# Optimization experiments

Measured on AMD Instinct MI355X. Metric: run time of the kernel, lower is better.

## Reference

```python
import jax, jax.numpy as jnp
import numpy as np

IMG, P, CIN, D, NH, NB, NC = 512, 16, 3, 384, 4, 3, 2
HD = D // NH
NP_ = (IMG // P) ** 2
T = NP_ + 1
FF = 4 * D


def _ln(x, s, b, eps=1e-5):
    m = x.mean(-1, keepdims=True)
    v = ((x - m) ** 2).mean(-1, keepdims=True)
    return (x - m) / jnp.sqrt(v + eps) * s + b


def setup_inputs() -> dict:
    key = jax.random.key(0)
    ks = jax.random.split(key, 20)
    s = 0.02
    inp = {
        'x': jax.random.normal(ks[0], (16, CIN, IMG, IMG), jnp.float32),
        'targets': jax.random.randint(ks[1], (16,), 0, NC),
        'conv_w': jax.random.normal(ks[2], (D, CIN, P, P), jnp.float32) * s,
        'conv_b': jnp.zeros((D,), jnp.float32),
        'cls_token': jax.random.normal(ks[3], (1, 1, D), jnp.float32),
        'pos_emb': jax.random.normal(ks[4], (T, D), jnp.float32) * s,
        'ln1_s': jnp.ones((NB, D), jnp.float32), 'ln1_b': jnp.zeros((NB, D), jnp.float32),
        'ln2_s': jnp.ones((NB, D), jnp.float32), 'ln2_b': jnp.zeros((NB, D), jnp.float32),
        'wq': jax.random.normal(ks[5], (NB, D, D), jnp.float32) * s,
        'wk': jax.random.normal(ks[6], (NB, D, D), jnp.float32) * s,
        'wv': jax.random.normal(ks[7], (NB, D, D), jnp.float32) * s,
        'wo': jax.random.normal(ks[8], (NB, D, D), jnp.float32) * s,
        'bo': jnp.zeros((NB, D), jnp.float32),
        'w1': jax.random.normal(ks[9], (NB, D, FF), jnp.float32) * s,
        'b1': jnp.zeros((NB, FF), jnp.float32),
        'w2': jax.random.normal(ks[10], (NB, FF, D), jnp.float32) * s,
        'b2': jnp.zeros((NB, D), jnp.float32),
        'lnf_s': jnp.ones((D,), jnp.float32), 'lnf_b': jnp.zeros((D,), jnp.float32),
        'proj_w': jax.random.normal(ks[11], (D, NC), jnp.float32) * s,
        'proj_b': jnp.zeros((NC,), jnp.float32),
    }
    return inp


def _forward(x, conv_w, conv_b, cls_token, pos_emb, ln1_s, ln1_b, ln2_s, ln2_b,
             wq, wk, wv, wo, bo, w1, b1, w2, b2, lnf_s, lnf_b, proj_w, proj_b):
    B = x.shape[0]
    # patch embedding: conv with kernel==stride == non-overlapping patches
    xp = x.reshape(B, CIN, IMG // P, P, IMG // P, P)
    pe = jnp.einsum('bchpwq,dcpq->bhwd', xp, conv_w).reshape(B, NP_, D) + conv_b
    h = jnp.concatenate([jnp.broadcast_to(cls_token, (B, 1, D)), pe], axis=1)  # (B,T,D)
    h = h + pos_emb
    scale = HD ** (-0.5)
    for i in range(NB):
        hn = _ln(h, ln1_s[i], ln1_b[i])
        q = (hn @ wq[i]).reshape(B, T, NH, HD).transpose(0, 2, 1, 3)
        k = (hn @ wk[i]).reshape(B, T, NH, HD).transpose(0, 2, 1, 3)
        v = (hn @ wv[i]).reshape(B, T, NH, HD).transpose(0, 2, 1, 3)
        # cdist p=2 (Euclidean distance) attention scores
        d2 = (jnp.sum(q * q, -1)[..., :, None] + jnp.sum(k * k, -1)[..., None, :]
              - 2.0 * jnp.einsum('bhqd,bhkd->bhqk', q, k))
        wei = jax.nn.softmax(jnp.sqrt(jnp.maximum(d2, 0.0)) * scale, axis=-1)
        vals = jnp.einsum('bhqk,bhkd->bhqd', wei, v).transpose(0, 2, 1, 3).reshape(B, T, D)
        h = h + vals @ wo[i] + bo[i]
        hn2 = _ln(h, ln2_s[i], ln2_b[i])
        h = h + jax.nn.relu(hn2 @ w1[i] + b1[i]) @ w2[i] + b2[i]
    h = _ln(h, lnf_s, lnf_b)
    logits = h @ proj_w + proj_b
    return logits[:, 0]  # (B, NC) cls-token logits


def reference(x, targets, conv_w, conv_b, cls_token, pos_emb, ln1_s, ln1_b, ln2_s, ln2_b,
              wq, wk, wv, wo, bo, w1, b1, w2, b2, lnf_s, lnf_b, proj_w, proj_b):
    cls_logits = _forward(x, conv_w, conv_b, cls_token, pos_emb, ln1_s, ln1_b, ln2_s, ln2_b,
                          wq, wk, wv, wo, bo, w1, b1, w2, b2, lnf_s, lnf_b, proj_w, proj_b)
    logp = jax.nn.log_softmax(cls_logits, axis=-1)
    loss = -jnp.mean(jnp.take_along_axis(logp, targets[:, None], axis=1))
    return (cls_logits, loss)
```

## Files before the change

### kernel.cpp

```cpp
#include <hip/hip_runtime.h>
#include <math.h>


#define BATCH   16
#define TSEQ    1025
#define DMODEL  384
#define NHEAD   4
#define HDIM    96
#define NBLK    3
#define FFDIM   1536
#define IMGSZ   512
#define NPATCHI 1024
#define MROWS   (BATCH*TSEQ)
#define MPATCH  (BATCH*NPATCHI)
#define KPE     768
#define VTS     1088
#define ATT_SCALE 0.10206207261596577f

typedef __attribute__((ext_vector_type(8))) __bf16 bf16x8;
typedef __attribute__((ext_vector_type(4))) float  f32x4;

__device__ __forceinline__ f32x4 fzero4() {
  f32x4 v; v[0] = 0.f; v[1] = 0.f; v[2] = 0.f; v[3] = 0.f; return v;
}
__device__ __forceinline__ bf16x8 bzero8() {
  bf16x8 v;
#pragma unroll
  for (int j = 0; j < 8; ++j) v[j] = (__bf16)0.f;
  return v;
}

template<int EPI>
__global__ __launch_bounds__(256, 2) void mgemm_k(
    const __bf16* __restrict__ A, const __bf16* __restrict__ Bt,
    const float* __restrict__ bias, const float* __restrict__ res,
    float* __restrict__ Cf, __bf16* __restrict__ Cb, int M, int N, int K)
{
  __shared__ __bf16 Al[2][128][40];
  __shared__ __bf16 Bl[2][128][40];
  const int tid = threadIdx.x;
  const int lane = tid & 63;
  const int w = tid >> 6;
  const int wr = w >> 1, wc = w & 1;
  const int l15 = lane & 15, g = lane >> 4;
  const int row0 = blockIdx.x * 128, col0 = blockIdx.y * 128;
  const int srow = tid >> 1, soff = (tid & 1) * 16;
  int ar = row0 + srow; if (ar > M - 1) ar = M - 1;
  const __bf16* ap = A + (size_t)ar * K + soff;
  const __bf16* bp = Bt + (size_t)(col0 + srow) * K + soff;

  f32x4 acc[4][4];
#pragma unroll
  for (int i = 0; i < 4; ++i)
#pragma unroll
    for (int j = 0; j < 4; ++j) acc[i][j] = fzero4();

  const int nk = K >> 5;
  bf16x8 ra0 = *(const bf16x8*)ap;
  bf16x8 ra1 = *(const bf16x8*)(ap + 8);
  bf16x8 rb0 = *(const bf16x8*)bp;
  bf16x8 rb1 = *(const bf16x8*)(bp + 8);
  *(bf16x8*)&Al[0][srow][soff]     = ra0;
  *(bf16x8*)&Al[0][srow][soff + 8] = ra1;
  *(bf16x8*)&Bl[0][srow][soff]     = rb0;
  *(bf16x8*)&Bl[0][srow][soff + 8] = rb1;
  __syncthreads();
  int cur = 0;
  for (int kt = 0; kt < nk; ++kt) {
    const bool pf = (kt + 1 < nk);
    if (pf) {
      const __bf16* a2 = ap + (size_t)(kt + 1) * 32;
      const __bf16* b2 = bp + (size_t)(kt + 1) * 32;
      ra0 = *(const bf16x8*)a2; ra1 = *(const bf16x8*)(a2 + 8);
      rb0 = *(const bf16x8*)b2; rb1 = *(const bf16x8*)(b2 + 8);
    }
    bf16x8 af[4], bfr[4];
#pragma unroll
    for (int mi = 0; mi < 4; ++mi)
      af[mi] = *(const bf16x8*)&Al[cur][wr * 64 + mi * 16 + l15][g * 8];
#pragma unroll
    for (int ni = 0; ni < 4; ++ni)
      bfr[ni] = *(const bf16x8*)&Bl[cur][wc * 64 + ni * 16 + l15][g * 8];
#pragma unroll
    for (int mi = 0; mi < 4; ++mi)
#pragma unroll
      for (int ni = 0; ni < 4; ++ni)
        acc[mi][ni] = __builtin_amdgcn_mfma_f32_16x16x32_bf16(
            af[mi], bfr[ni], acc[mi][ni], 0, 0, 0);
    if (pf) {
      *(bf16x8*)&Al[cur ^ 1][srow][soff]     = ra0;
      *(bf16x8*)&Al[cur ^ 1][srow][soff + 8] = ra1;
      *(bf16x8*)&Bl[cur ^ 1][srow][soff]     = rb0;
      *(bf16x8*)&Bl[cur ^ 1][srow][soff + 8] = rb1;
    }
    __syncthreads();
    cur ^= 1;
  }
#pragma unroll
  for (int ni = 0; ni < 4; ++ni) {
    const int gc = col0 + wc * 64 + ni * 16 + l15;
    const float bv = (EPI & 1) ? bias[gc] : 0.f;
#pragma unroll
    for (int mi = 0; mi < 4; ++mi) {
#pragma unroll
      for (int r = 0; r < 4; ++r) {
        const int gr = row0 + wr * 64 + mi * 16 + g * 4 + r;
        if (gr >= M) continue;
        float v = acc[mi][ni][r] + bv;
        if (EPI & 2) v = fmaxf(v, 0.f);
        if (EPI & 4) v += res[(size_t)gr * N + gc];
        if (EPI & 8)  Cf[(size_t)gr * N + gc] = v;
        if (EPI & 16) Cb[(size_t)gr * N + gc] = (__bf16)v;
      }
    }
  }
}

__global__ void vtr_k(const __bf16* __restrict__ qkv, __bf16* __restrict__ Vt)
{
  __shared__ __bf16 t[32][33];
  const int bh = blockIdx.z;
  const int bb = bh >> 2, hh = bh & 3;
  const int t0 = blockIdx.x * 32;
  const int d0 = blockIdx.y * 32;
  const int tx = threadIdx.x, ty = threadIdx.y;
#pragma unroll
  for (int i = 0; i < 4; ++i) {
    const int tt = t0 + ty + 8 * i;
    t[ty + 8 * i][tx] = (tt < TSEQ)
        ? qkv[(size_t)(bb * TSEQ + tt) * 1152 + 768 + hh * 96 + d0 + tx]
        : (__bf16)0.f;
  }
  __syncthreads();
#pragma unroll
  for (int i = 0; i < 4; ++i)
    Vt[((size_t)bh * 96 + d0 + ty + 8 * i) * VTS + t0 + tx] = t[tx][ty + 8 * i];
}

__global__ __launch_bounds__(256, 4) void attn_k(
    const __bf16* __restrict__ qkv, const __bf16* __restrict__ Vtg,
    const float* __restrict__ sq2, const float* __restrict__ sk2,
    __bf16* __restrict__ O)
{
  __shared__ __bf16 Kl[64][104];
  __shared__ __bf16 Vl[96][72];
  __shared__ __bf16 Pl[64][72];
  const int qt = blockIdx.x, bh = blockIdx.y;
  const int bb = bh >> 2, hh = bh & 3;
  const int tid = threadIdx.x;
  const int w = tid >> 6, lane = tid & 63;
  const int l15 = lane & 15, g = lane >> 4;
  const int q0 = qt * 64 + w * 16;
  const float* sq2h = sq2 + (size_t)bh * TSEQ;
  const float* sk2h = sk2 + (size_t)bh * TSEQ;
  const __bf16* vbase = Vtg + (size_t)bh * 96 * VTS;

  bf16x8 qf[3];
  float sqv[4];
  {
    int qr = q0 + l15; if (qr > TSEQ - 1) qr = TSEQ - 1;
    const __bf16* qp = qkv + (size_t)(bb * TSEQ + qr) * 1152 + hh * 96 + g * 8;
#pragma unroll
    for (int kf = 0; kf < 3; ++kf) qf[kf] = *(const bf16x8*)(qp + kf * 32);
#pragma unroll
    for (int r = 0; r < 4; ++r) {
      int qq = q0 + g * 4 + r; if (qq > TSEQ - 1) qq = TSEQ - 1;
      sqv[r] = sq2h[qq];
    }
  }

  float mrun[4], lrun[4];
  f32x4 accO[6];
#pragma unroll
  for (int r = 0; r < 4; ++r) { mrun[r] = -INFINITY; lrun[r] = 0.f; }
#pragma unroll
  for (int n = 0; n < 6; ++n) accO[n] = fzero4();

  bf16x8 kr[3], vr[3];
  auto load_chunk = [&](int c) {
    const int kbase = c * 64;
#pragma unroll
    for (int i = 0; i < 3; ++i) {
      const int idx = tid + i * 256;
      const int row = idx / 12, cc = idx - row * 12;
      const int kg = kbase + row;
      kr[i] = (kg < TSEQ)
          ? *(const bf16x8*)(qkv + (size_t)(bb * TSEQ + kg) * 1152 + 384
                             + hh * 96 + cc * 8)
          : bzero8();
      const int d = idx >> 3, o8 = (idx & 7) * 8;
      vr[i] = *(const bf16x8*)(vbase + (size_t)d * VTS + kbase + o8);
    }
  };

  load_chunk(0);

  for (int c = 0; c < 17; ++c) {
    const int kbase = c * 64;
    __syncthreads();
#pragma unroll
    for (int i = 0; i < 3; ++i) {
      const int idx = tid + i * 256;
      const int row = idx / 12, cc = idx - row * 12;
      *(bf16x8*)&Kl[row][cc * 8] = kr[i];
      const int d = idx >> 3, o8 = (idx & 7) * 8;
      *(bf16x8*)&Vl[d][o8] = vr[i];
    }
    __syncthreads();
    if (c + 1 < 17) load_chunk(c + 1);

    f32x4 sf[4];
#pragma unroll
    for (int ks = 0; ks < 4; ++ks) sf[ks] = fzero4();
    __builtin_amdgcn_s_setprio(1);
#pragma unroll
    for (int ks = 0; ks < 4; ++ks) {
      bf16x8 kb0 = *(const bf16x8*)&Kl[ks * 16 + l15][g * 8];
      bf16x8 kb1 = *(const bf16x8*)&Kl[ks * 16 + l15][32 + g * 8];
      bf16x8 kb2 = *(const bf16x8*)&Kl[ks * 16 + l15][64 + g * 8];
      sf[ks] = __builtin_amdgcn_mfma_f32_16x16x32_bf16(qf[0], kb0, sf[ks], 0, 0, 0);
      sf[ks] = __builtin_amdgcn_mfma_f32_16x16x32_bf16(qf[1], kb1, sf[ks], 0, 0, 0);
      sf[ks] = __builtin_amdgcn_mfma_f32_16x16x32_bf16(qf[2], kb2, sf[ks], 0, 0, 0);
    }
    __builtin_amdgcn_s_setprio(0);

    float nmax[4] = {-INFINITY, -INFINITY, -INFINITY, -INFINITY};
#pragma unroll
    for (int ks = 0; ks < 4; ++ks) {
      const int kgl = kbase + ks * 16 + l15;
      const bool kvld = (kgl < TSEQ);
      const float kv2 = sk2h[kvld ? kgl : 0];
#pragma unroll
      for (int r = 0; r < 4; ++r) {
        const float d2 = sqv[r] + kv2 - 2.f * sf[ks][r];
        const float s = kvld ? sqrtf(fmaxf(d2, 0.f)) * ATT_SCALE : -INFINITY;
        sf[ks][r] = s;
        nmax[r] = fmaxf(nmax[r], s);
      }
    }
#pragma unroll
    for (int r = 0; r < 4; ++r) {
      float v = nmax[r];
      v = fmaxf(v, __shfl_xor(v, 1, 64));
      v = fmaxf(v, __shfl_xor(v, 2, 64));
      v = fmaxf(v, __shfl_xor(v, 4, 64));
      v = fmaxf(v, __shfl_xor(v, 8, 64));
      const float mn = fmaxf(mrun[r], v);
      const float f = __expf(mrun[r] - mn);
      mrun[r] = mn;
      lrun[r] *= f;
#pragma unroll
      for (int n = 0; n < 6; ++n) accO[n][r] *= f;
    }
    float ps[4] = {0.f, 0.f, 0.f, 0.f};
#pragma unroll
    for (int ks = 0; ks < 4; ++ks)
#pragma unroll
      for (int r = 0; r < 4; ++r) {
        const float p = __expf(sf[ks][r] - mrun[r]);
        ps[r] += p;
        Pl[w * 16 + g * 4 + r][ks * 16 + l15] = (__bf16)p;
      }
#pragma unroll
    for (int r = 0; r < 4; ++r) {
      float v = ps[r];
      v += __shfl_xor(v, 1, 64);
      v += __shfl_xor(v, 2, 64);
      v += __shfl_xor(v, 4, 64);
      v += __shfl_xor(v, 8, 64);
      lrun[r] += v;
    }

    __builtin_amdgcn_s_setprio(1);
#pragma unroll
    for (int ks2 = 0; ks2 < 2; ++ks2) {
      bf16x8 pa = *(const bf16x8*)&Pl[w * 16 + l15][ks2 * 32 + g * 8];
#pragma unroll
      for (int n = 0; n < 6; ++n) {
        bf16x8 vb = *(const bf16x8*)&Vl[n * 16 + l15][ks2 * 32 + g * 8];
        accO[n] = __builtin_amdgcn_mfma_f32_16x16x32_bf16(pa, vb, accO[n], 0, 0, 0);
      }
    }
    __builtin_amdgcn_s_setprio(0);
  }

#pragma unroll
  for (int r = 0; r < 4; ++r) {
    const int qr = q0 + g * 4 + r;
    if (qr >= TSEQ) continue;
    const float inv = 1.f / lrun[r];
#pragma unroll
    for (int n = 0; n < 6; ++n)
      O[(size_t)(bb * TSEQ + qr) * 384 + hh * 96 + n * 16 + l15] =
          (__bf16)(accO[n][r] * inv);
  }
}

__global__ __launch_bounds__(256) void im2col_k(
    const float* __restrict__ x, __bf16* __restrict__ Ai)
{
  const int i = blockIdx.x * 256 + threadIdx.x;
  const int row = i / 96;
  const int k = (i - row * 96) * 8;
  const int b = row >> 10;
  const int pidx = row & 1023;
  const int py = pidx >> 5, px = pidx & 31;
  const int cc = k >> 8;
  const int rem = k & 255;
  const int p = rem >> 4, q = rem & 15;
  const float* src = x + ((size_t)((b * 3 + cc) * IMGSZ + py * 16 + p)) * IMGSZ
                       + px * 16 + q;
  const float4 a = *(const float4*)src;
  const float4 c4 = *(const float4*)(src + 4);
  bf16x8 o;
  o[0] = (__bf16)a.x;  o[1] = (__bf16)a.y;  o[2] = (__bf16)a.z;  o[3] = (__bf16)a.w;
  o[4] = (__bf16)c4.x; o[5] = (__bf16)c4.y; o[6] = (__bf16)c4.z; o[7] = (__bf16)c4.w;
  *(bf16x8*)&Ai[(size_t)i * 8] = o;
}

__global__ void wt_k(const float* __restrict__ src, size_t srcZ,
                     __bf16* __restrict__ dst, size_t dstZ, int K, int N)
{
  __shared__ float t[32][33];
  const float* s = src + blockIdx.z * srcZ;
  __bf16* d = dst + blockIdx.z * dstZ;
  const int k0 = blockIdx.x * 32, n0 = blockIdx.y * 32;
  const int tx = threadIdx.x, ty = threadIdx.y;
#pragma unroll
  for (int i = 0; i < 4; ++i)
    t[ty + 8 * i][tx] = s[(size_t)(k0 + ty + 8 * i) * N + n0 + tx];
  __syncthreads();
#pragma unroll
  for (int i = 0; i < 4; ++i)
    d[(size_t)(n0 + ty + 8 * i) * K + k0 + tx] = (__bf16)t[tx][ty + 8 * i];
}

__global__ void cvt_k(const float* __restrict__ src, __bf16* __restrict__ dst, int n8)
{
  const int i = blockIdx.x * 256 + threadIdx.x;
  if (i >= n8) return;
  const float4 a = *(const float4*)&src[(size_t)i * 8];
  const float4 b = *(const float4*)&src[(size_t)i * 8 + 4];
  bf16x8 o;
  o[0] = (__bf16)a.x; o[1] = (__bf16)a.y; o[2] = (__bf16)a.z; o[3] = (__bf16)a.w;
  o[4] = (__bf16)b.x; o[5] = (__bf16)b.y; o[6] = (__bf16)b.z; o[7] = (__bf16)b.w;
  *(bf16x8*)&dst[(size_t)i * 8] = o;
}

__global__ __launch_bounds__(256) void embed_k(
    const float* __restrict__ pe, const float* __restrict__ cls,
    const float* __restrict__ pos, float* __restrict__ h)
{
  const int i = blockIdx.x * 256 + threadIdx.x;
  const int row = i / 96;
  const int d4 = (i - row * 96) * 4;
  const int b = row / TSEQ;
  const int t = row - b * TSEQ;
  const float4 po = *(const float4*)&pos[(size_t)t * DMODEL + d4];
  float4 r;
  if (t == 0) {
    const float4 cv = *(const float4*)&cls[d4];
    r = make_float4(cv.x + po.x, cv.y + po.y, cv.z + po.z, cv.w + po.w);
  } else {
    const float4 pv = *(const float4*)&pe[((size_t)(b * NPATCHI + t - 1)) * DMODEL + d4];
    r = make_float4(pv.x + po.x, pv.y + po.y, pv.z + po.z, pv.w + po.w);
  }
  *(float4*)&h[(size_t)row * DMODEL + d4] = r;
}

__global__ __launch_bounds__(256) void ln_k(
    const float* __restrict__ in, const float* __restrict__ sc,
    const float* __restrict__ bi, __bf16* __restrict__ out)
{
  const int w = threadIdx.x >> 6, lane = threadIdx.x & 63;
  const int row = blockIdx.x * 4 + w;
  const float* r = in + (size_t)row * DMODEL;
  float v[6], sum = 0.f, ss = 0.f;
#pragma unroll
  for (int j = 0; j < 6; ++j) {
    const float xv = r[lane + 64 * j];
    v[j] = xv; sum += xv; ss += xv * xv;
  }
#pragma unroll
  for (int m = 1; m < 64; m <<= 1) {
    sum += __shfl_xor(sum, m, 64);
    ss  += __shfl_xor(ss,  m, 64);
  }
  const float mean = sum * (1.f / 384.f);
  const float var  = ss * (1.f / 384.f) - mean * mean;
  const float rstd = rsqrtf(var + 1e-5f);
  __bf16* o = out + (size_t)row * DMODEL;
#pragma unroll
  for (int j = 0; j < 6; ++j) {
    const int col = lane + 64 * j;
    o[col] = (__bf16)((v[j] - mean) * rstd * sc[col] + bi[col]);
  }
}

__global__ __launch_bounds__(256) void sumsq_k(
    const __bf16* __restrict__ qkv, float* __restrict__ sq2,
    float* __restrict__ sk2)
{
  const int w = threadIdx.x >> 6, lane = threadIdx.x & 63;
  const int row = blockIdx.x * 4 + w;
  const int h = lane >> 4, lg = lane & 15;
  const __bf16* q = qkv + (size_t)row * 1152 + h * HDIM;
  float s1 = 0.f, s2 = 0.f;
#pragma unroll
  for (int j = 0; j < 6; ++j) {
    const float a = (float)q[lg + 16 * j];
    const float c = (float)q[384 + lg + 16 * j];
    s1 += a * a; s2 += c * c;
  }
#pragma unroll
  for (int m = 1; m < 16; m <<= 1) {
    s1 += __shfl_xor(s1, m, 64);
    s2 += __shfl_xor(s2, m, 64);
  }
  if (lg == 0) {
    const int b = row / TSEQ, t = row - b * TSEQ;
    sq2[((size_t)b * NHEAD + h) * TSEQ + t] = s1;
    sk2[((size_t)b * NHEAD + h) * TSEQ + t] = s2;
  }
}

__global__ __launch_bounds__(256) void head_k(
    const float* __restrict__ h, const float* __restrict__ gs,
    const float* __restrict__ gb, const float* __restrict__ pw,
    const float* __restrict__ pb, const int* __restrict__ tgt,
    float* __restrict__ out)
{
  __shared__ float lg[BATCH][2];
  const int w = threadIdx.x >> 6, lane = threadIdx.x & 63;
  for (int b = w; b < BATCH; b += 4) {
    const float* r = h + (size_t)b * TSEQ * DMODEL;
    float v[6], sum = 0.f, ss = 0.f;
#pragma unroll
    for (int j = 0; j < 6; ++j) {
      const float xv = r[lane + 64 * j];
      v[j] = xv; sum += xv; ss += xv * xv;
    }
#pragma unroll
    for (int m = 1; m < 64; m <<= 1) {
      sum += __shfl_xor(sum, m, 64);
      ss  += __shfl_xor(ss,  m, 64);
    }
    const float mean = sum * (1.f / 384.f);
    const float var  = ss * (1.f / 384.f) - mean * mean;
    const float rstd = rsqrtf(var + 1e-5f);
    float l0 = 0.f, l1 = 0.f;
#pragma unroll
    for (int j = 0; j < 6; ++j) {
      const int col = lane + 64 * j;
      const float hnv = (v[j] - mean) * rstd * gs[col] + gb[col];
      l0 = fmaf(hnv, pw[col * 2 + 0], l0);
      l1 = fmaf(hnv, pw[col * 2 + 1], l1);
    }
#pragma unroll
    for (int m = 1; m < 64; m <<= 1) {
      l0 += __shfl_xor(l0, m, 64);
      l1 += __shfl_xor(l1, m, 64);
    }
    if (lane == 0) { lg[b][0] = l0 + pb[0]; lg[b][1] = l1 + pb[1]; }
  }
  __syncthreads();
  if (threadIdx.x < 32)
    out[threadIdx.x] = lg[threadIdx.x >> 1][threadIdx.x & 1];
  if (threadIdx.x == 0) {
    float acc = 0.f;
    for (int b = 0; b < BATCH; ++b) {
      const float a = lg[b][0], c = lg[b][1];
      const float mx = fmaxf(a, c);
      const float lse = mx + logf(expf(a - mx) + expf(c - mx));
      const float lp = ((tgt[b] == 0) ? a : c) - lse;
      acc += lp;
    }
    out[32] = -acc * (1.f / BATCH);
  }
}

extern "C" void kernel_launch(void* const* d_in, const int* in_sizes, int n_in,
                              void* d_out, int out_size, void* d_ws, size_t ws_size,
                              hipStream_t stream)
{
  const float* x       = (const float*)d_in[0];
  const int*   targets = (const int*)  d_in[1];
  const float* conv_w  = (const float*)d_in[2];
  const float* conv_b  = (const float*)d_in[3];
  const float* cls_tok = (const float*)d_in[4];
  const float* pos_emb = (const float*)d_in[5];
  const float* ln1_s   = (const float*)d_in[6];
  const float* ln1_b   = (const float*)d_in[7];
  const float* ln2_s   = (const float*)d_in[8];
  const float* ln2_b   = (const float*)d_in[9];
  const float* wq      = (const float*)d_in[10];
  const float* wk      = (const float*)d_in[11];
  const float* wv      = (const float*)d_in[12];
  const float* wo      = (const float*)d_in[13];
  const float* bo      = (const float*)d_in[14];
  const float* w1      = (const float*)d_in[15];
  const float* b1      = (const float*)d_in[16];
  const float* w2      = (const float*)d_in[17];
  const float* b2      = (const float*)d_in[18];
  const float* lnf_s   = (const float*)d_in[19];
  const float* lnf_b   = (const float*)d_in[20];
  const float* proj_w  = (const float*)d_in[21];
  const float* proj_b  = (const float*)d_in[22];

  char* p = (char*)d_ws;
  auto alloc = [&](size_t bytes) -> void* {
    void* r = (void*)p; p += (bytes + 255) & ~(size_t)255; return r;
  };
  float*  h     = (float*) alloc((size_t)MROWS * DMODEL * 4);
  __bf16* hn    = (__bf16*)alloc((size_t)MROWS * DMODEL * 2);
  __bf16* qkv   = (__bf16*)alloc((size_t)MROWS * 1152 * 2);
  __bf16* Obuf  = (__bf16*)alloc((size_t)MROWS * DMODEL * 2);
  float*  pe    = (float*) alloc((size_t)MPATCH * DMODEL * 4);
  float*  sq2   = (float*) alloc((size_t)BATCH * NHEAD * TSEQ * 4);
  float*  sk2   = (float*) alloc((size_t)BATCH * NHEAD * TSEQ * 4);
  __bf16* cwb   = (__bf16*)alloc((size_t)DMODEL * KPE * 2);
  __bf16* wqkvT = (__bf16*)alloc((size_t)NBLK * 1152 * DMODEL * 2);
  __bf16* woT   = (__bf16*)alloc((size_t)NBLK * DMODEL * DMODEL * 2);
  __bf16* w1T   = (__bf16*)alloc((size_t)NBLK * FFDIM * DMODEL * 2);
  __bf16* w2T   = (__bf16*)alloc((size_t)NBLK * DMODEL * FFDIM * 2);
  if ((size_t)(p - (char*)d_ws) > ws_size) return;
  __bf16* Ai  = qkv;
  __bf16* ffb = qkv;
  __bf16* Vtg = (__bf16*)pe;

  cvt_k<<<144, 256, 0, stream>>>(conv_w, cwb, (DMODEL * KPE) / 8);
  {
    dim3 blk(32, 8);
    wt_k<<<dim3(12, 12, 3), blk, 0, stream>>>(wq, (size_t)DMODEL * DMODEL,
        wqkvT + 0,               (size_t)1152 * DMODEL, DMODEL, DMODEL);
    wt_k<<<dim3(12, 12, 3), blk, 0, stream>>>(wk, (size_t)DMODEL * DMODEL,
        wqkvT + 384 * DMODEL,    (size_t)1152 * DMODEL, DMODEL, DMODEL);
    wt_k<<<dim3(12, 12, 3), blk, 0, stream>>>(wv, (size_t)DMODEL * DMODEL,
        wqkvT + 768 * DMODEL,    (size_t)1152 * DMODEL, DMODEL, DMODEL);
    wt_k<<<dim3(12, 12, 3), blk, 0, stream>>>(wo, (size_t)DMODEL * DMODEL,
        woT, (size_t)DMODEL * DMODEL, DMODEL, DMODEL);
    wt_k<<<dim3(12, 48, 3), blk, 0, stream>>>(w1, (size_t)DMODEL * FFDIM,
        w1T, (size_t)FFDIM * DMODEL, DMODEL, FFDIM);
    wt_k<<<dim3(48, 12, 3), blk, 0, stream>>>(w2, (size_t)FFDIM * DMODEL,
        w2T, (size_t)DMODEL * FFDIM, FFDIM, DMODEL);
  }

  im2col_k<<<6144, 256, 0, stream>>>(x, Ai);
  mgemm_k<9><<<dim3(128, 3), 256, 0, stream>>>(
      Ai, cwb, conv_b, nullptr, pe, nullptr, MPATCH, DMODEL, KPE);
  embed_k<<<6150, 256, 0, stream>>>(pe, cls_tok, pos_emb, h);

  for (int i = 0; i < NBLK; ++i) {
    ln_k<<<4100, 256, 0, stream>>>(h, ln1_s + i * DMODEL, ln1_b + i * DMODEL, hn);
    mgemm_k<16><<<dim3(129, 9), 256, 0, stream>>>(
        hn, wqkvT + (size_t)i * 1152 * DMODEL, nullptr, nullptr,
        nullptr, qkv, MROWS, 1152, DMODEL);
    sumsq_k<<<4100, 256, 0, stream>>>(qkv, sq2, sk2);
    vtr_k<<<dim3(34, 3, 64), dim3(32, 8), 0, stream>>>(qkv, Vtg);
    attn_k<<<dim3(17, 64), 256, 0, stream>>>(qkv, Vtg, sq2, sk2, Obuf);
    mgemm_k<13><<<dim3(129, 3), 256, 0, stream>>>(
        Obuf, woT + (size_t)i * DMODEL * DMODEL, bo + i * DMODEL, h,
        h, nullptr, MROWS, DMODEL, DMODEL);
    ln_k<<<4100, 256, 0, stream>>>(h, ln2_s + i * DMODEL, ln2_b + i * DMODEL, hn);
    mgemm_k<19><<<dim3(129, 12), 256, 0, stream>>>(
        hn, w1T + (size_t)i * FFDIM * DMODEL, b1 + i * FFDIM, nullptr,
        nullptr, ffb, MROWS, FFDIM, DMODEL);
    mgemm_k<13><<<dim3(129, 3), 256, 0, stream>>>(
        ffb, w2T + (size_t)i * DMODEL * FFDIM, b2 + i * DMODEL, h,
        h, nullptr, MROWS, DMODEL, FFDIM);
  }

  head_k<<<1, 256, 0, stream>>>(h, lnf_s, lnf_b, proj_w, proj_b, targets,
                                (float*)d_out);
}
```

Before: 1.296 ms.

## Use direct global-to-LDS loads in GEMM and register-fed lazy-rescale attention

The GEMM now stages tiles with global_load_lds straight into unpadded LDS, dropping the register round-trip, and raises occupancy to 4 blocks per SM. The attention kernel no longer stages K and V through LDS; each wave loads its K and V fragments from global memory into registers. Online softmax rescaling is skipped unless a row max grows by more than 8. The row sum comes from an appended ones-row in Vt, computed by a seventh MFMA column tile. The cost is redundant global traffic per wave and wasted MFMA work on the padding rows, and the unpadded LDS layout may cause bank conflicts. GEMM rows are no longer clamped to M, so the last partial tile reads past the end of A.

```diff
diff --git a/kernel.cpp b/kernel.cpp
--- a/kernel.cpp
+++ b/kernel.cpp
@@ -15,39 +15,41 @@
 #define MPATCH  (BATCH*NPATCHI)
 #define KPE     768
 #define VTS     1088
+#define VROWS   112
 #define ATT_SCALE 0.10206207261596577f
 
 typedef __attribute__((ext_vector_type(8))) __bf16 bf16x8;
 typedef __attribute__((ext_vector_type(4))) float  f32x4;
+typedef unsigned int u32;
 
 __device__ __forceinline__ f32x4 fzero4() {
   f32x4 v; v[0] = 0.f; v[1] = 0.f; v[2] = 0.f; v[3] = 0.f; return v;
 }
-__device__ __forceinline__ bf16x8 bzero8() {
-  bf16x8 v;
-#pragma unroll
-  for (int j = 0; j < 8; ++j) v[j] = (__bf16)0.f;
-  return v;
+
+__device__ __forceinline__ void gl_lds16(const __bf16* g, __bf16* l) {
+  __builtin_amdgcn_global_load_lds(
+      (const __attribute__((address_space(1))) u32*)g,
+      (__attribute__((address_space(3))) u32*)l, 16, 0, 0);
 }
 
 template<int EPI>
-__global__ __launch_bounds__(256, 2) void mgemm_k(
+__global__ __launch_bounds__(256, 4) void mgemm_k(
     const __bf16* __restrict__ A, const __bf16* __restrict__ Bt,
     const float* __restrict__ bias, const float* __restrict__ res,
     float* __restrict__ Cf, __bf16* __restrict__ Cb, int M, int N, int K)
 {
-  __shared__ __bf16 Al[2][128][40];
-  __shared__ __bf16 Bl[2][128][40];
+  __shared__ __bf16 Al[2][128][32];
+  __shared__ __bf16 Bl[2][128][32];
   const int tid = threadIdx.x;
   const int lane = tid & 63;
   const int w = tid >> 6;
   const int wr = w >> 1, wc = w & 1;
   const int l15 = lane & 15, g = lane >> 4;
   const int row0 = blockIdx.x * 128, col0 = blockIdx.y * 128;
-  const int srow = tid >> 1, soff = (tid & 1) * 16;
-  int ar = row0 + srow; if (ar > M - 1) ar = M - 1;
-  const __bf16* ap = A + (size_t)ar * K + soff;
-  const __bf16* bp = Bt + (size_t)(col0 + srow) * K + soff;
+  const int sr = w * 32 + (lane >> 2);
+  const int sc = (lane & 3) * 8;
+  const __bf16* Ab = A  + (size_t)(row0 + sr) * K + sc;
+  const __bf16* Bb = Bt + (size_t)(col0 + sr) * K + sc;
 
   f32x4 acc[4][4];
 #pragma unroll
@@ -56,24 +58,19 @@
     for (int j = 0; j < 4; ++j) acc[i][j] = fzero4();
 
   const int nk = K >> 5;
-  bf16x8 ra0 = *(const bf16x8*)ap;
-  bf16x8 ra1 = *(const bf16x8*)(ap + 8);
-  bf16x8 rb0 = *(const bf16x8*)bp;
-  bf16x8 rb1 = *(const bf16x8*)(bp + 8);
-  *(bf16x8*)&Al[0][srow][soff]     = ra0;
-  *(bf16x8*)&Al[0][srow][soff + 8] = ra1;
-  *(bf16x8*)&Bl[0][srow][soff]     = rb0;
-  *(bf16x8*)&Bl[0][srow][soff + 8] = rb1;
+  auto stage = [&](int buf, int kt) {
+#pragma unroll
+    for (int j = 0; j < 2; ++j) {
+      gl_lds16(Ab + (size_t)(j * 16) * K + kt * 32, &Al[buf][w * 32 + j * 16][0]);
+      gl_lds16(Bb + (size_t)(j * 16) * K + kt * 32, &Bl[buf][w * 32 + j * 16][0]);
+    }
+  };
+
+  stage(0, 0);
   __syncthreads();
   int cur = 0;
   for (int kt = 0; kt < nk; ++kt) {
-    const bool pf = (kt + 1 < nk);
-    if (pf) {
-      const __bf16* a2 = ap + (size_t)(kt + 1) * 32;
-      const __bf16* b2 = bp + (size_t)(kt + 1) * 32;
-      ra0 = *(const bf16x8*)a2; ra1 = *(const bf16x8*)(a2 + 8);
-      rb0 = *(const bf16x8*)b2; rb1 = *(const bf16x8*)(b2 + 8);
-    }
+    if (kt + 1 < nk) stage(cur ^ 1, kt + 1);
     bf16x8 af[4], bfr[4];
 #pragma unroll
     for (int mi = 0; mi < 4; ++mi)
@@ -81,18 +78,14 @@
 #pragma unroll
     for (int ni = 0; ni < 4; ++ni)
       bfr[ni] = *(const bf16x8*)&Bl[cur][wc * 64 + ni * 16 + l15][g * 8];
+    __builtin_amdgcn_s_setprio(1);
 #pragma unroll
     for (int mi = 0; mi < 4; ++mi)
 #pragma unroll
       for (int ni = 0; ni < 4; ++ni)
         acc[mi][ni] = __builtin_amdgcn_mfma_f32_16x16x32_bf16(
             af[mi], bfr[ni], acc[mi][ni], 0, 0, 0);
-    if (pf) {
-      *(bf16x8*)&Al[cur ^ 1][srow][soff]     = ra0;
-      *(bf16x8*)&Al[cur ^ 1][srow][soff + 8] = ra1;
-      *(bf16x8*)&Bl[cur ^ 1][srow][soff]     = rb0;
-      *(bf16x8*)&Bl[cur ^ 1][srow][soff + 8] = rb1;
-    }
+    __builtin_amdgcn_s_setprio(0);
     __syncthreads();
     cur ^= 1;
   }
@@ -124,6 +117,16 @@
   const int t0 = blockIdx.x * 32;
   const int d0 = blockIdx.y * 32;
   const int tx = threadIdx.x, ty = threadIdx.y;
+  if (d0 >= 96) {
+#pragma unroll
+    for (int i = 0; i < 4; ++i) {
+      const int d = d0 + ty + 8 * i;
+      if (d < VROWS)
+        Vt[((size_t)bh * VROWS + d) * VTS + t0 + tx] =
+            (d == 96) ? (__bf16)1.f : (__bf16)0.f;
+    }
+    return;
+  }
 #pragma unroll
   for (int i = 0; i < 4; ++i) {
     const int tt = t0 + ty + 8 * i;
@@ -134,16 +137,14 @@
   __syncthreads();
 #pragma unroll
   for (int i = 0; i < 4; ++i)
-    Vt[((size_t)bh * 96 + d0 + ty + 8 * i) * VTS + t0 + tx] = t[tx][ty + 8 * i];
-}
-
-__global__ __launch_bounds__(256, 4) void attn_k(
+    Vt[((size_t)bh * VROWS + d0 + ty + 8 * i) * VTS + t0 + tx] = t[tx][ty + 8 * i];
+}
+
+__global__ __launch_bounds__(256, 3) void attn_k(
     const __bf16* __restrict__ qkv, const __bf16* __restrict__ Vtg,
     const float* __restrict__ sq2, const float* __restrict__ sk2,
     __bf16* __restrict__ O)
 {
-  __shared__ __bf16 Kl[64][104];
-  __shared__ __bf16 Vl[96][72];
   __shared__ __bf16 Pl[64][72];
   const int qt = blockIdx.x, bh = blockIdx.y;
   const int bb = bh >> 2, hh = bh & 3;
@@ -153,7 +154,8 @@
   const int q0 = qt * 64 + w * 16;
   const float* sq2h = sq2 + (size_t)bh * TSEQ;
   const float* sk2h = sk2 + (size_t)bh * TSEQ;
-  const __bf16* vbase = Vtg + (size_t)bh * 96 * VTS;
+  const __bf16* kbp = qkv + (size_t)bb * TSEQ * 1152 + 384 + hh * 96;
+  const __bf16* vbp = Vtg + (size_t)bh * VROWS * VTS;
 
   bf16x8 qf[3];
   float sqv[4];
@@ -169,62 +171,44 @@
     }
   }
 
-  float mrun[4], lrun[4];
-  f32x4 accO[6];
-#pragma unroll
-  for (int r = 0; r < 4; ++r) { mrun[r] = -INFINITY; lrun[r] = 0.f; }
-#pragma unroll
-  for (int n = 0; n < 6; ++n) accO[n] = fzero4();
-
-  bf16x8 kr[3], vr[3];
-  auto load_chunk = [&](int c) {
-    const int kbase = c * 64;
-#pragma unroll
-    for (int i = 0; i < 3; ++i) {
-      const int idx = tid + i * 256;
-      const int row = idx / 12, cc = idx - row * 12;
-      const int kg = kbase + row;
-      kr[i] = (kg < TSEQ)
-          ? *(const bf16x8*)(qkv + (size_t)(bb * TSEQ + kg) * 1152 + 384
-                             + hh * 96 + cc * 8)
-          : bzero8();
-      const int d = idx >> 3, o8 = (idx & 7) * 8;
-      vr[i] = *(const bf16x8*)(vbase + (size_t)d * VTS + kbase + o8);
-    }
-  };
-
-  load_chunk(0);
+  float mrun[4];
+  f32x4 accO[7];
+#pragma unroll
+  for (int r = 0; r < 4; ++r) mrun[r] = -INFINITY;
+#pragma unroll
+  for (int n = 0; n < 7; ++n) accO[n] = fzero4();
 
   for (int c = 0; c < 17; ++c) {
     const int kbase = c * 64;
-    __syncthreads();
-#pragma unroll
-    for (int i = 0; i < 3; ++i) {
-      const int idx = tid + i * 256;
-      const int row = idx / 12, cc = idx - row * 12;
-      *(bf16x8*)&Kl[row][cc * 8] = kr[i];
-      const int d = idx >> 3, o8 = (idx & 7) * 8;
-      *(bf16x8*)&Vl[d][o8] = vr[i];
-    }
-    __syncthreads();
-    if (c + 1 < 17) load_chunk(c + 1);
 
     f32x4 sf[4];
 #pragma unroll
     for (int ks = 0; ks < 4; ++ks) sf[ks] = fzero4();
-    __builtin_amdgcn_s_setprio(1);
-#pragma unroll
-    for (int ks = 0; ks < 4; ++ks) {
-      bf16x8 kb0 = *(const bf16x8*)&Kl[ks * 16 + l15][g * 8];
-      bf16x8 kb1 = *(const bf16x8*)&Kl[ks * 16 + l15][32 + g * 8];
-      bf16x8 kb2 = *(const bf16x8*)&Kl[ks * 16 + l15][64 + g * 8];
-      sf[ks] = __builtin_amdgcn_mfma_f32_16x16x32_bf16(qf[0], kb0, sf[ks], 0, 0, 0);
-      sf[ks] = __builtin_amdgcn_mfma_f32_16x16x32_bf16(qf[1], kb1, sf[ks], 0, 0, 0);
-      sf[ks] = __builtin_amdgcn_mfma_f32_16x16x32_bf16(qf[2], kb2, sf[ks], 0, 0, 0);
-    }
-    __builtin_amdgcn_s_setprio(0);
-
-    float nmax[4] = {-INFINITY, -INFINITY, -INFINITY, -INFINITY};
+    {
+      bf16x8 kb[4][3];
+#pragma unroll
+      for (int ks = 0; ks < 4; ++ks) {
+        int krow = kbase + ks * 16 + l15; if (krow > TSEQ - 1) krow = TSEQ - 1;
+        const __bf16* kp = kbp + (size_t)krow * 1152 + g * 8;
+#pragma unroll
+        for (int kf = 0; kf < 3; ++kf) kb[ks][kf] = *(const bf16x8*)(kp + kf * 32);
+      }
+      __builtin_amdgcn_s_setprio(1);
+#pragma unroll
+      for (int ks = 0; ks < 4; ++ks)
+#pragma unroll
+        for (int kf = 0; kf < 3; ++kf)
+          sf[ks] = __builtin_amdgcn_mfma_f32_16x16x32_bf16(
+              qf[kf], kb[ks][kf], sf[ks], 0, 0, 0);
+      __builtin_amdgcn_s_setprio(0);
+    }
+
+    bf16x8 vb0[7];
+#pragma unroll
+    for (int n = 0; n < 7; ++n)
+      vb0[n] = *(const bf16x8*)(vbp + (size_t)(n * 16 + l15) * VTS + kbase + g * 8);
+
+    float cm[4] = {-INFINITY, -INFINITY, -INFINITY, -INFINITY};
 #pragma unroll
     for (int ks = 0; ks < 4; ++ks) {
       const int kgl = kbase + ks * 16 + l15;
@@ -235,52 +219,47 @@
         const float d2 = sqv[r] + kv2 - 2.f * sf[ks][r];
         const float s = kvld ? sqrtf(fmaxf(d2, 0.f)) * ATT_SCALE : -INFINITY;
         sf[ks][r] = s;
-        nmax[r] = fmaxf(nmax[r], s);
+        cm[r] = fmaxf(cm[r], s);
       }
     }
-#pragma unroll
-    for (int r = 0; r < 4; ++r) {
-      float v = nmax[r];
-      v = fmaxf(v, __shfl_xor(v, 1, 64));
-      v = fmaxf(v, __shfl_xor(v, 2, 64));
-      v = fmaxf(v, __shfl_xor(v, 4, 64));
-      v = fmaxf(v, __shfl_xor(v, 8, 64));
-      const float mn = fmaxf(mrun[r], v);
-      const float f = __expf(mrun[r] - mn);
-      mrun[r] = mn;
-      lrun[r] *= f;
-#pragma unroll
-      for (int n = 0; n < 6; ++n) accO[n][r] *= f;
-    }
-    float ps[4] = {0.f, 0.f, 0.f, 0.f};
+
+    const bool okl = (cm[0] <= mrun[0] + 8.f) && (cm[1] <= mrun[1] + 8.f) &&
+                     (cm[2] <= mrun[2] + 8.f) && (cm[3] <= mrun[3] + 8.f);
+    if (!__all(okl)) {
+#pragma unroll
+      for (int r = 0; r < 4; ++r) {
+        float v = cm[r];
+        v = fmaxf(v, __shfl_xor(v, 1, 64));
+        v = fmaxf(v, __shfl_xor(v, 2, 64));
+        v = fmaxf(v, __shfl_xor(v, 4, 64));
+        v = fmaxf(v, __shfl_xor(v, 8, 64));
+        const float mn = fmaxf(mrun[r], v);
+        const float f = __expf(mrun[r] - mn);
+        mrun[r] = mn;
+#pragma unroll
+        for (int n = 0; n < 7; ++n) accO[n][r] *= f;
+      }
+    }
+
 #pragma unroll
     for (int ks = 0; ks < 4; ++ks)
 #pragma unroll
-      for (int r = 0; r < 4; ++r) {
-        const float p = __expf(sf[ks][r] - mrun[r]);
-        ps[r] += p;
-        Pl[w * 16 + g * 4 + r][ks * 16 + l15] = (__bf16)p;
-      }
-#pragma unroll
-    for (int r = 0; r < 4; ++r) {
-      float v = ps[r];
-      v += __shfl_xor(v, 1, 64);
-      v += __shfl_xor(v, 2, 64);
-      v += __shfl_xor(v, 4, 64);
-      v += __shfl_xor(v, 8, 64);
-      lrun[r] += v;
-    }
-
+      for (int r = 0; r < 4; ++r)
+        Pl[w * 16 + g * 4 + r][ks * 16 + l15] = (__bf16)__expf(sf[ks][r] - mrun[r]);
+
+    bf16x8 vb1[7];
+#pragma unroll
+    for (int n = 0; n < 7; ++n)
+      vb1[n] = *(const bf16x8*)(vbp + (size_t)(n * 16 + l15) * VTS + kbase + 32 + g * 8);
+    bf16x8 pa0 = *(const bf16x8*)&Pl[w * 16 + l15][g * 8];
+    bf16x8 pa1 = *(const bf16x8*)&Pl[w * 16 + l15][32 + g * 8];
     __builtin_amdgcn_s_setprio(1);
 #pragma unroll
-    for (int ks2 = 0; ks2 < 2; ++ks2) {
-      bf16x8 pa = *(const bf16x8*)&Pl[w * 16 + l15][ks2 * 32 + g * 8];
-#pragma unroll
-      for (int n = 0; n < 6; ++n) {
-        bf16x8 vb = *(const bf16x8*)&Vl[n * 16 + l15][ks2 * 32 + g * 8];
-        accO[n] = __builtin_amdgcn_mfma_f32_16x16x32_bf16(pa, vb, accO[n], 0, 0, 0);
-      }
-    }
+    for (int n = 0; n < 7; ++n)
+      accO[n] = __builtin_amdgcn_mfma_f32_16x16x32_bf16(pa0, vb0[n], accO[n], 0, 0, 0);
+#pragma unroll
+    for (int n = 0; n < 7; ++n)
+      accO[n] = __builtin_amdgcn_mfma_f32_16x16x32_bf16(pa1, vb1[n], accO[n], 0, 0, 0);
     __builtin_amdgcn_s_setprio(0);
   }
 
@@ -288,7 +267,8 @@
   for (int r = 0; r < 4; ++r) {
     const int qr = q0 + g * 4 + r;
     if (qr >= TSEQ) continue;
-    const float inv = 1.f / lrun[r];
+    const float lr = __shfl(accO[6][r], lane & 48, 64);
+    const float inv = 1.f / lr;
 #pragma unroll
     for (int n = 0; n < 6; ++n)
       O[(size_t)(bb * TSEQ + qr) * 384 + hh * 96 + n * 16 + l15] =
@@ -556,7 +536,7 @@
         hn, wqkvT + (size_t)i * 1152 * DMODEL, nullptr, nullptr,
         nullptr, qkv, MROWS, 1152, DMODEL);
     sumsq_k<<<4100, 256, 0, stream>>>(qkv, sq2, sk2);
-    vtr_k<<<dim3(34, 3, 64), dim3(32, 8), 0, stream>>>(qkv, Vtg);
+    vtr_k<<<dim3(34, 4, 64), dim3(32, 8), 0, stream>>>(qkv, Vtg);
     attn_k<<<dim3(17, 64), 256, 0, stream>>>(qkv, Vtg, sq2, sk2, Obuf);
     mgemm_k<13><<<dim3(129, 3), 256, 0, stream>>>(
         Obuf, woT + (size_t)i * DMODEL * DMODEL, bo + i * DMODEL, h,
```

Measured after the change: 1.530 ms. +18.0%, slower.
